# Kernel tuning notes

Hardware: AMD Instinct MI355X
Metric: run time of the kernel (lower is better)

The kernel has to match this reference:

```python
import jax, jax.numpy as jnp
import numpy as np

B, L, E, H, CDIM = 512, 64, 256, 256, 64
NEG = -1e9  # stand-in for -inf mask fill (keeps grads nan-free; probs underflow to 0)
C_EXPL = 10.0  # tanh_exploration


def setup_inputs():
    key = jax.random.key(0)
    ks = jax.random.split(key, 24)
    rn = lambda k, s: jax.random.normal(k, s, jnp.float32) * 0.05
    return {
        'decoder_input': rn(ks[0], (B, E)),
        'embedded_inputs': rn(ks[1], (L, B, E)),
        'h0': rn(ks[2], (B, H)),
        'c0': rn(ks[3], (B, H)),
        'context': rn(ks[4], (L, B, H)),
        'courier_fea': rn(ks[5], (B, CDIM)),
        'init_mask': jnp.zeros((B, L), dtype=bool),
        # LSTMCell params (torch gate order i,f,g,o)
        'W_ih': rn(ks[6], (4 * H, E)), 'W_hh': rn(ks[7], (4 * H, H)),
        'b_ih': rn(ks[8], (4 * H,)), 'b_hh': rn(ks[9], (4 * H,)),
        # merge_linear
        'Wm': rn(ks[10], (H, H + CDIM)), 'bm': rn(ks[11], (H,)),
        # pointer attention
        'Wq_p': rn(ks[12], (H, H)), 'bq_p': rn(ks[13], (H,)),
        'Wr_p': rn(ks[14], (H, H)), 'br_p': rn(ks[15], (H,)),
        'v_p': rn(ks[16], (H,)),
        # glimpse attention
        'Wq_g': rn(ks[17], (H, H)), 'bq_g': rn(ks[18], (H,)),
        'Wr_g': rn(ks[19], (H, H)), 'br_g': rn(ks[20], (H,)),
        'v_g': rn(ks[21], (H,)),
    }


def _attn_scores(q_lin, e, v, use_tanh):
    # q_lin: [B,H], e: [B,H,L], v: [H] -> u: [B,L]
    u = jnp.einsum('h,bhl->bl', v, jnp.tanh(q_lin[:, :, None] + e))
    return C_EXPL * jnp.tanh(u) if use_tanh else u


def _forward(decoder_input, embedded_inputs, h0, c0, context, courier_fea,
             W_ih, W_hh, b_ih, b_hh, Wm, bm,
             Wq_p, bq_p, Wr_p, br_p, v_p,
             Wq_g, bq_g, Wr_g, br_g, v_g, init_mask):
    Ln, Bn = context.shape[0], context.shape[1]
    # conv1d(kernel=1) projection of encoder refs; constant over steps -> precompute
    e_g = jnp.einsum('oh,lbh->bol', Wr_g, context) + br_g[None, :, None]  # [B,H,L]
    e_p = jnp.einsum('oh,lbh->bol', Wr_p, context) + br_p[None, :, None]
    rows = jnp.arange(Bn)

    def update_mask(mask, sel):
        m = mask.at[rows, sel].set(True)
        all_true = m.all(axis=1)
        return m.at[:, -1].set(jnp.where(all_true, False, m[:, -1]))

    def step(carry, t):
        h, c, mask, idxs, x = carry
        mask = jnp.where(t == 0, mask, update_mask(mask, jnp.clip(idxs, 0)))
        # LSTMCell
        gates = x @ W_ih.T + b_ih + h @ W_hh.T + b_hh
        i_, f_, g_, o_ = jnp.split(gates, 4, axis=1)
        c = jax.nn.sigmoid(f_) * c + jax.nn.sigmoid(i_) * jnp.tanh(g_)
        h = jax.nn.sigmoid(o_) * jnp.tanh(c)
        # merge hidden with courier features
        gl = jnp.concatenate([h, courier_fea], axis=1) @ Wm.T + bm
        # one glimpse (n_glimpses=1), masked
        lg = _attn_scores(gl @ Wq_g.T + bq_g, e_g, v_g, use_tanh=False)
        lg = jnp.where(mask, NEG, lg)
        gl = jnp.einsum('bhl,bl->bh', e_g, jax.nn.softmax(lg, axis=1))
        # pointer logits (C*tanh), masked
        lp = _attn_scores(gl @ Wq_p.T + bq_p, e_p, v_p, use_tanh=True)
        lp = jnp.where(mask, NEG, lp)
        log_p = jax.nn.log_softmax(lp, axis=1)  # [B,L]
        new_idxs = jnp.argmax(log_p, axis=1).astype(jnp.int32)  # greedy decode
        new_x = embedded_inputs[new_idxs, rows, :]  # gather next input [B,E]
        return (h, c, mask, new_idxs, new_x), (log_p, new_idxs)

    init = (h0, c0, init_mask, jnp.full((Bn,), -1, jnp.int32), decoder_input)
    _, (log_ps, sels) = jax.lax.scan(step, init, jnp.arange(Ln))
    return jnp.swapaxes(log_ps, 0, 1), jnp.swapaxes(sels, 0, 1)  # [B,L,L], [B,L]


def reference(decoder_input, embedded_inputs, h0, c0, context, courier_fea, init_mask,
              W_ih, W_hh, b_ih, b_hh, Wm, bm,
              Wq_p, bq_p, Wr_p, br_p, v_p,
              Wq_g, bq_g, Wr_g, br_g, v_g):
    return _forward(decoder_input, embedded_inputs, h0, c0, context, courier_fea,
                    W_ih, W_hh, b_ih, b_hh, Wm, bm,
                    Wq_p, bq_p, Wr_p, br_p, v_p,
                    Wq_g, bq_g, Wr_g, br_g, v_g, init_mask)
```

## Files before the change

### kernel.cpp

```cpp
#include <hip/hip_runtime.h>
#include <cstdint>
#include <cstddef>

#define NEGV -1000000000.0f

__device__ __forceinline__ float fsigm(float x) {
  return 1.0f / (1.0f + __expf(-x));
}
__device__ __forceinline__ float ftanh(float x) {
  x = fminf(x, 30.0f);
  const float e = __expf(2.0f * x);
  return (e - 1.0f) / (e + 1.0f);
}

__global__ __launch_bounds__(256, 2) void gemm2_k(
    const float* __restrict__ A0, const float* __restrict__ W2,
    const float* __restrict__ b2, float* __restrict__ Cg,
    float* __restrict__ Cp)
{
  __shared__ float As[16][136];
  __shared__ float Ws[2][16][72];
  const int bn = blockIdx.x << 6;
  const int bm = blockIdx.y << 7;
  const int t  = threadIdx.x;
  const int ty = t >> 4, tx = t & 15;
  const int ar = t >> 1, ac = (t & 1) << 3;
  const int wr = t >> 2, wc = (t & 3) << 2;
  const float* arow = A0 + (size_t)(bm + ar) * 256 + ac;
  float acc[2][8][4] = {};
  for (int k0 = 0; k0 < 256; k0 += 16) {
    const float4 a0 = *(const float4*)(arow + k0);
    const float4 a1 = *(const float4*)(arow + k0 + 4);
    As[ac + 0][ar] = a0.x; As[ac + 1][ar] = a0.y; As[ac + 2][ar] = a0.z; As[ac + 3][ar] = a0.w;
    As[ac + 4][ar] = a1.x; As[ac + 5][ar] = a1.y; As[ac + 6][ar] = a1.z; As[ac + 7][ar] = a1.w;
#pragma unroll
    for (int s = 0; s < 2; ++s) {
      const float4 wv = *(const float4*)(W2 + (size_t)(s * 256 + bn + wr) * 256 + k0 + wc);
      Ws[s][wc + 0][wr] = wv.x; Ws[s][wc + 1][wr] = wv.y;
      Ws[s][wc + 2][wr] = wv.z; Ws[s][wc + 3][wr] = wv.w;
    }
    __syncthreads();
#pragma unroll
    for (int k = 0; k < 16; ++k) {
      const float4 a0v = *(const float4*)&As[k][ty << 3];
      const float4 a1v = *(const float4*)&As[k][(ty << 3) + 4];
      const float am[8] = {a0v.x, a0v.y, a0v.z, a0v.w, a1v.x, a1v.y, a1v.z, a1v.w};
#pragma unroll
      for (int s = 0; s < 2; ++s) {
        const float4 wv = *(const float4*)&Ws[s][k][tx << 2];
#pragma unroll
        for (int i = 0; i < 8; ++i) {
          acc[s][i][0] += am[i] * wv.x;
          acc[s][i][1] += am[i] * wv.y;
          acc[s][i][2] += am[i] * wv.z;
          acc[s][i][3] += am[i] * wv.w;
        }
      }
    }
    __syncthreads();
  }
  const int cn = bn + (tx << 2);
  const float4 bg = *(const float4*)(b2 + cn);
  const float4 bp = *(const float4*)(b2 + 256 + cn);
#pragma unroll
  for (int i = 0; i < 8; ++i) {
    const size_t row = ((size_t)(bm + (ty << 3) + i)) << 8;
    float4 o;
    o.x = acc[0][i][0] + bg.x; o.y = acc[0][i][1] + bg.y;
    o.z = acc[0][i][2] + bg.z; o.w = acc[0][i][3] + bg.w;
    *(float4*)(Cg + row + cn) = o;
    o.x = acc[1][i][0] + bp.x; o.y = acc[1][i][1] + bp.y;
    o.z = acc[1][i][2] + bp.z; o.w = acc[1][i][3] + bp.w;
    *(float4*)(Cp + row + cn) = o;
  }
}

__global__ __launch_bounds__(256) void gates_lstm_k(
    const float* __restrict__ x, const float* __restrict__ hin,
    const float* __restrict__ Wcat, const float* __restrict__ bcat,
    const float* __restrict__ cin, float* __restrict__ cnew,
    float* __restrict__ hnew)
{
  __shared__ __align__(16) float As[16][36];
  __shared__ __align__(16) float Ws[32][68];
  const int bn = blockIdx.x << 6;
  const int bm = blockIdx.y << 4;
  const int t  = threadIdx.x;
  const int ty = t >> 4, tx = t & 15;
  const int ar = t >> 4, ak = (t & 15) << 1;
  const int wr = t >> 2, wk = (t & 3) << 3;
  const float* wrow = Wcat + ((size_t)(bn + wr) << 9);
  const int arow = bm + ar;
  float acc0 = 0.f, acc1 = 0.f, acc2 = 0.f, acc3 = 0.f;
  for (int k0 = 0; k0 < 512; k0 += 32) {
    const int kk = k0 + ak;
    float2 av;
    if (kk < 256) av = *(const float2*)(x   + ((size_t)arow << 8) + kk);
    else          av = *(const float2*)(hin + ((size_t)arow << 8) + (kk - 256));
    const float4 w0 = *(const float4*)(wrow + k0 + wk);
    const float4 w1 = *(const float4*)(wrow + k0 + wk + 4);
    *(float2*)&As[ar][ak] = av;
    Ws[wk + 0][wr] = w0.x; Ws[wk + 1][wr] = w0.y; Ws[wk + 2][wr] = w0.z; Ws[wk + 3][wr] = w0.w;
    Ws[wk + 4][wr] = w1.x; Ws[wk + 5][wr] = w1.y; Ws[wk + 6][wr] = w1.z; Ws[wk + 7][wr] = w1.w;
    __syncthreads();
#pragma unroll
    for (int k = 0; k < 32; ++k) {
      const float a  = As[ty][k];
      const float4 w = *(const float4*)&Ws[k][tx << 2];
      acc0 += a * w.x; acc1 += a * w.y; acc2 += a * w.z; acc3 += a * w.w;
    }
    __syncthreads();
  }
  const float4 bb = *(const float4*)(bcat + bn + (tx << 2));
  const int jc = (bn >> 2) + tx;
  const int m  = bm + ty;
  const float ig = fsigm(acc0 + bb.x);
  const float fg = fsigm(acc1 + bb.y);
  const float gg = ftanh(acc2 + bb.z);
  const float og = fsigm(acc3 + bb.w);
  const float c  = fg * cin[(m << 8) + jc] + ig * gg;
  const float h  = og * ftanh(c);
  cnew[(m << 8) + jc] = c;
  hnew[(m << 8) + jc] = h;
}

__global__ __launch_bounds__(512) void step_attn_k(
    const float* __restrict__ h, const float* __restrict__ e2g,
    const float* __restrict__ e2p, const float* __restrict__ Wq1T4,
    const float* __restrict__ Wqp4, const float* __restrict__ qcour,
    const float* __restrict__ bqp, const float* __restrict__ vg,
    const float* __restrict__ vp, unsigned long long* __restrict__ mask,
    int* __restrict__ idxb, const float* __restrict__ emb,
    float* __restrict__ out_logp, float* __restrict__ out_sel,
    float* __restrict__ xb, int t)
{
  const int b = blockIdx.x, tid = threadIdx.x;
  __shared__ __align__(16) float hs[256], qgs[256], qps[256], gls[256];
  __shared__ __align__(16) float vgs[256], vps[256];
  __shared__ __align__(16) float glp[8][256];
  __shared__ __align__(16) float part[512];
  __shared__ float us[64], mxs[8], zws[8];
  __shared__ unsigned long long ms;
  __shared__ int bsel;
  if (tid < 256) {
    hs[tid]  = h[(b << 8) + tid];
    vgs[tid] = vg[tid];
    vps[tid] = vp[tid];
  }
  if (tid == 0) {
    unsigned long long m = mask[b];
    if (t > 0) {
      int s = idxb[b]; if (s < 0) s = 0;
      m |= (1ULL << s);
      if (m == ~0ULL) m &= ~(1ULL << 63);
      mask[b] = m;
    }
    ms = m;
  }
  __syncthreads();
  const unsigned long long mm = ms;
  const int w = tid >> 6, lane = tid & 63;
  const int o = tid & 255, kh = tid >> 8;

  {
    float acc = (kh == 0) ? qcour[(b << 8) + o] : 0.f;
    const float4* wp = (const float4*)Wq1T4 + o;
    const int kc0 = kh << 5;
#pragma unroll 8
    for (int kc = kc0; kc < kc0 + 32; ++kc) {
      const float4 wv = wp[kc << 8];
      const float4 h4 = *(const float4*)&hs[kc << 2];
      acc += wv.x * h4.x + wv.y * h4.y + wv.z * h4.z + wv.w * h4.w;
    }
    part[tid] = acc;
  }
  __syncthreads();
  if (tid < 256) qgs[tid] = part[tid] + part[tid + 256];
  __syncthreads();

  {
    const float4 q4 = *(const float4*)&qgs[lane << 2];
    const float4 v4 = *(const float4*)&vgs[lane << 2];
    const float* ebase = e2g + ((size_t)b << 8) + (lane << 2);
    float g0 = 0.f, g1 = 0.f, g2 = 0.f, g3 = 0.f;
    float mxw = -1e30f, zw = 0.f;
    for (int li = 0; li < 8; ++li) {
      const int l = (w << 3) + li;
      const float4 e4 = *(const float4*)(ebase + ((size_t)l << 17));
      float s = v4.x * ftanh(q4.x + e4.x) + v4.y * ftanh(q4.y + e4.y)
              + v4.z * ftanh(q4.z + e4.z) + v4.w * ftanh(q4.w + e4.w);
#pragma unroll
      for (int off = 32; off; off >>= 1) s += __shfl_xor(s, off, 64);
      if (!((mm >> l) & 1ULL)) {
        const float nm   = fmaxf(mxw, s);
        const float corr = __expf(mxw - nm);
        const float wl   = __expf(s - nm);
        zw = zw * corr + wl;
        g0 = g0 * corr + wl * e4.x; g1 = g1 * corr + wl * e4.y;
        g2 = g2 * corr + wl * e4.z; g3 = g3 * corr + wl * e4.w;
        mxw = nm;
      }
    }
    glp[w][(lane << 2) + 0] = g0; glp[w][(lane << 2) + 1] = g1;
    glp[w][(lane << 2) + 2] = g2; glp[w][(lane << 2) + 3] = g3;
    if (lane == 0) { mxs[w] = mxw; zws[w] = zw; }
  }
  __syncthreads();
  if (tid < 256) {
    float MX = mxs[0];
#pragma unroll
    for (int ww = 1; ww < 8; ++ww) MX = fmaxf(MX, mxs[ww]);
    float Z = 0.f, go = 0.f;
#pragma unroll
    for (int ww = 0; ww < 8; ++ww) {
      const float sc = __expf(mxs[ww] - MX);
      Z  += sc * zws[ww];
      go += sc * glp[ww][tid];
    }
    gls[tid] = go / Z;
  }
  __syncthreads();

  {
    float acc = (kh == 0) ? bqp[o] : 0.f;
    const float4* wp = (const float4*)Wqp4 + o;
    const int kc0 = kh << 5;
#pragma unroll 8
    for (int kc = kc0; kc < kc0 + 32; ++kc) {
      const float4 wv = wp[kc << 8];
      const float4 h4 = *(const float4*)&gls[kc << 2];
      acc += wv.x * h4.x + wv.y * h4.y + wv.z * h4.z + wv.w * h4.w;
    }
    part[tid] = acc;
  }
  __syncthreads();
  if (tid < 256) qps[tid] = part[tid] + part[tid + 256];
  __syncthreads();

  {
    const float4 q4 = *(const float4*)&qps[lane << 2];
    const float4 v4 = *(const float4*)&vps[lane << 2];
    const float* ebase = e2p + ((size_t)b << 8) + (lane << 2);
    for (int li = 0; li < 8; ++li) {
      const int l = (w << 3) + li;
      const float4 e4 = *(const float4*)(ebase + ((size_t)l << 17));
      float s = v4.x * ftanh(q4.x + e4.x) + v4.y * ftanh(q4.y + e4.y)
              + v4.z * ftanh(q4.z + e4.z) + v4.w * ftanh(q4.w + e4.w);
#pragma unroll
      for (int off = 32; off; off >>= 1) s += __shfl_xor(s, off, 64);
      if (lane == 0) us[l] = ((mm >> l) & 1ULL) ? NEGV : 10.0f * ftanh(s);
    }
  }
  __syncthreads();
  if (tid < 64) {
    const float xv = us[tid];
    float mx = xv;
#pragma unroll
    for (int off = 32; off; off >>= 1) mx = fmaxf(mx, __shfl_xor(mx, off, 64));
    const float sh = xv - mx;
    const float ev = __expf(sh);
    float sum = ev;
#pragma unroll
    for (int off = 32; off; off >>= 1) sum += __shfl_xor(sum, off, 64);
    const float lp = sh - __logf(sum);
    out_logp[((size_t)b << 12) + (t << 6) + tid] = lp;
    float bv = lp; int bi = tid;
#pragma unroll
    for (int off = 32; off; off >>= 1) {
      const float ov = __shfl_xor(bv, off, 64);
      const int   oi = __shfl_xor(bi, off, 64);
      if (ov > bv || (ov == bv && oi < bi)) { bv = ov; bi = oi; }
    }
    if (tid == 0) { idxb[b] = bi; out_sel[(b << 6) + t] = (float)bi; bsel = bi; }
  }
  __syncthreads();
  if (tid < 256) xb[(b << 8) + tid] = emb[(((size_t)(bsel << 9) + b) << 8) + tid];
}

__global__ __launch_bounds__(256) void init_k(
    const float* __restrict__ dec, const float* __restrict__ h0,
    const float* __restrict__ c0, float* __restrict__ xb,
    float* __restrict__ hb, float* __restrict__ cb,
    unsigned long long* __restrict__ mask, int* __restrict__ idxb)
{
  const int i = blockIdx.x * 256 + threadIdx.x;
  xb[i] = dec[i]; hb[i] = h0[i]; cb[i] = c0[i];
  if (i < 512) { mask[i] = 0ULL; idxb[i] = -1; }
}

__global__ __launch_bounds__(256) void prep_wcat_k(
    const float* __restrict__ Wih, const float* __restrict__ Whh,
    const float* __restrict__ bih, const float* __restrict__ bhh,
    float* __restrict__ Wcat, float* __restrict__ bcat)
{
  const int id = blockIdx.x * 256 + threadIdx.x;
  const int n = id >> 9, k = id & 511;
  const int r = ((n & 3) << 8) + (n >> 2);
  Wcat[id] = (k < 256) ? Wih[(r << 8) + k] : Whh[(r << 8) + (k - 256)];
  if (id < 1024) {
    const int rr = ((id & 3) << 8) + (id >> 2);
    bcat[id] = bih[rr] + bhh[rr];
  }
}

__global__ __launch_bounds__(256) void prep_wfused_k(
    const float* __restrict__ Wqg, const float* __restrict__ Wm,
    const float* __restrict__ bm, const float* __restrict__ bqg,
    float* __restrict__ Wf, float* __restrict__ bf)
{
  const int id = blockIdx.x * 256 + threadIdx.x;
  const int o = id / 320, j = id % 320;
  float acc = 0.f;
  for (int tt = 0; tt < 256; ++tt) acc += Wqg[(o << 8) + tt] * Wm[tt * 320 + j];
  Wf[id] = acc;
  if (id < 256) {
    float a2 = 0.f;
    for (int tt = 0; tt < 256; ++tt) a2 += Wqg[(id << 8) + tt] * bm[tt];
    bf[id] = a2 + bqg[id];
  }
}

__global__ __launch_bounds__(256) void prep_wq1t4_k(
    const float* __restrict__ Wf, float* __restrict__ Wq1T4)
{
  const int id = blockIdx.x * 256 + threadIdx.x;
  const int k = id >> 8, o = id & 255;
  Wq1T4[((k >> 2) << 10) + (o << 2) + (k & 3)] = Wf[o * 320 + k];
}

__global__ __launch_bounds__(256) void prep_wqp4_k(
    const float* __restrict__ Wqp, float* __restrict__ Wqp4)
{
  const int id = blockIdx.x * 256 + threadIdx.x;
  const int k = id >> 8, o = id & 255;
  Wqp4[((k >> 2) << 10) + (o << 2) + (k & 3)] = Wqp[(o << 8) + k];
}

__global__ __launch_bounds__(256) void prep_qcour_k(
    const float* __restrict__ Wf, const float* __restrict__ bf,
    const float* __restrict__ cour, float* __restrict__ qcour)
{
  const int b = blockIdx.x, o = threadIdx.x;
  __shared__ float cs[64];
  if (o < 64) cs[o] = cour[(b << 6) + o];
  __syncthreads();
  float acc = bf[o];
#pragma unroll 8
  for (int k = 0; k < 64; ++k) acc += Wf[o * 320 + 256 + k] * cs[k];
  qcour[(b << 8) + o] = acc;
}

__global__ __launch_bounds__(256) void prep_w2copy_k(
    const float* __restrict__ Wrg, const float* __restrict__ Wrp,
    const float* __restrict__ brg, const float* __restrict__ brp,
    float* __restrict__ W2, float* __restrict__ b2)
{
  const int id = blockIdx.x * 256 + threadIdx.x;
  W2[id] = (id < 65536) ? Wrg[id] : Wrp[id - 65536];
  if (id < 256) b2[id] = brg[id];
  else if (id < 512) b2[id] = brp[id - 256];
}

extern "C" void kernel_launch(void* const* d_in, const int* in_sizes, int n_in,
                              void* d_out, int out_size, void* d_ws, size_t ws_size,
                              hipStream_t stream)
{
  const float* dec   = (const float*)d_in[0];
  const float* emb   = (const float*)d_in[1];
  const float* h0    = (const float*)d_in[2];
  const float* c0    = (const float*)d_in[3];
  const float* ctxin = (const float*)d_in[4];
  const float* cour  = (const float*)d_in[5];
  const float* Wih   = (const float*)d_in[7];
  const float* Whh   = (const float*)d_in[8];
  const float* bih   = (const float*)d_in[9];
  const float* bhh   = (const float*)d_in[10];
  const float* Wm    = (const float*)d_in[11];
  const float* bm    = (const float*)d_in[12];
  const float* Wqp   = (const float*)d_in[13];
  const float* bqp   = (const float*)d_in[14];
  const float* Wrp   = (const float*)d_in[15];
  const float* brp   = (const float*)d_in[16];
  const float* vp    = (const float*)d_in[17];
  const float* Wqg   = (const float*)d_in[18];
  const float* bqg   = (const float*)d_in[19];
  const float* Wrg   = (const float*)d_in[20];
  const float* brg   = (const float*)d_in[21];
  const float* vg    = (const float*)d_in[22];

  float* ws = (float*)d_ws;
  float* e2g    = ws + 0;
  float* e2p    = ws + 8388608;
  float* W2     = ws + 16777216;
  float* b2     = ws + 16908288;
  float* Wcat   = ws + 16908800;
  float* bcat   = ws + 17433088;
  float* Wfused = ws + 17434112;
  float* bfused = ws + 17516032;
  float* Wq1T4  = ws + 17516288;
  float* Wqp4   = ws + 17581824;
  float* qcour  = ws + 17647360;
  float* hb0    = ws + 17778432;
  float* hb1    = ws + 17909504;
  float* cb0    = ws + 18040576;
  float* cb1    = ws + 18171648;
  float* xb     = ws + 18302720;
  unsigned long long* maskb = (unsigned long long*)(ws + 18433792);
  int* idxb     = (int*)(ws + 18434816);

  float* out_logp = (float*)d_out;
  float* out_sel  = (float*)d_out + 2097152;

  init_k<<<512, 256, 0, stream>>>(dec, h0, c0, xb, hb0, cb0, maskb, idxb);
  prep_wcat_k<<<2048, 256, 0, stream>>>(Wih, Whh, bih, bhh, Wcat, bcat);
  prep_wfused_k<<<320, 256, 0, stream>>>(Wqg, Wm, bm, bqg, Wfused, bfused);
  prep_wq1t4_k<<<256, 256, 0, stream>>>(Wfused, Wq1T4);
  prep_wqp4_k<<<256, 256, 0, stream>>>(Wqp, Wqp4);
  prep_qcour_k<<<512, 256, 0, stream>>>(Wfused, bfused, cour, qcour);
  prep_w2copy_k<<<512, 256, 0, stream>>>(Wrg, Wrp, brg, brp, W2, b2);
  gemm2_k<<<dim3(4, 256), 256, 0, stream>>>(ctxin, W2, b2, e2g, e2p);

  for (int t = 0; t < 64; ++t) {
    float* hcur = (t & 1) ? hb1 : hb0;
    float* hnew = (t & 1) ? hb0 : hb1;
    float* ccur = (t & 1) ? cb1 : cb0;
    float* cnew = (t & 1) ? cb0 : cb1;
    gates_lstm_k<<<dim3(16, 32), 256, 0, stream>>>(xb, hcur, Wcat, bcat,
                                                   ccur, cnew, hnew);
    step_attn_k<<<512, 512, 0, stream>>>(hnew, e2g, e2p, Wq1T4, Wqp4, qcour,
                                         bqp, vg, vp, maskb, idxb, emb,
                                         out_logp, out_sel, xb, t);
  }
}
```

Before: 3.187 ms.

## Prefetch global loads into registers across GEMM tiles and attention phases

Both GEMM kernels now load the next k-tile from global memory into registers while the current tile is computed from shared memory, a register double-buffering scheme. The gemm2 grid is transposed so consecutive blocks walk the M dimension. The step attention kernel issues its e2g loads before the query matvec and its e2p loads before the glimpse reduction, so the memory latency overlaps earlier compute. This raises register pressure, which could reduce occupancy in the 512-thread attention kernel.

```diff
diff --git a/kernel.cpp b/kernel.cpp
--- a/kernel.cpp
+++ b/kernel.cpp
@@ -20,26 +20,34 @@
 {
   __shared__ float As[16][136];
   __shared__ float Ws[2][16][72];
-  const int bn = blockIdx.x << 6;
-  const int bm = blockIdx.y << 7;
+  const int bm = blockIdx.x << 7;
+  const int bn = blockIdx.y << 6;
   const int t  = threadIdx.x;
   const int ty = t >> 4, tx = t & 15;
   const int ar = t >> 1, ac = (t & 1) << 3;
   const int wr = t >> 2, wc = (t & 3) << 2;
   const float* arow = A0 + (size_t)(bm + ar) * 256 + ac;
+  const float* w0row = W2 + (size_t)(bn + wr) * 256 + wc;
+  const float* w1row = W2 + (size_t)(256 + bn + wr) * 256 + wc;
   float acc[2][8][4] = {};
+  float4 a0 = *(const float4*)(arow + 0);
+  float4 a1 = *(const float4*)(arow + 4);
+  float4 wv0 = *(const float4*)(w0row + 0);
+  float4 wv1 = *(const float4*)(w1row + 0);
   for (int k0 = 0; k0 < 256; k0 += 16) {
-    const float4 a0 = *(const float4*)(arow + k0);
-    const float4 a1 = *(const float4*)(arow + k0 + 4);
     As[ac + 0][ar] = a0.x; As[ac + 1][ar] = a0.y; As[ac + 2][ar] = a0.z; As[ac + 3][ar] = a0.w;
     As[ac + 4][ar] = a1.x; As[ac + 5][ar] = a1.y; As[ac + 6][ar] = a1.z; As[ac + 7][ar] = a1.w;
-#pragma unroll
-    for (int s = 0; s < 2; ++s) {
-      const float4 wv = *(const float4*)(W2 + (size_t)(s * 256 + bn + wr) * 256 + k0 + wc);
-      Ws[s][wc + 0][wr] = wv.x; Ws[s][wc + 1][wr] = wv.y;
-      Ws[s][wc + 2][wr] = wv.z; Ws[s][wc + 3][wr] = wv.w;
-    }
+    Ws[0][wc + 0][wr] = wv0.x; Ws[0][wc + 1][wr] = wv0.y;
+    Ws[0][wc + 2][wr] = wv0.z; Ws[0][wc + 3][wr] = wv0.w;
+    Ws[1][wc + 0][wr] = wv1.x; Ws[1][wc + 1][wr] = wv1.y;
+    Ws[1][wc + 2][wr] = wv1.z; Ws[1][wc + 3][wr] = wv1.w;
     __syncthreads();
+    if (k0 < 240) {
+      a0  = *(const float4*)(arow + k0 + 16);
+      a1  = *(const float4*)(arow + k0 + 20);
+      wv0 = *(const float4*)(w0row + k0 + 16);
+      wv1 = *(const float4*)(w1row + k0 + 16);
+    }
 #pragma unroll
     for (int k = 0; k < 16; ++k) {
       const float4 a0v = *(const float4*)&As[k][ty << 3];
@@ -91,18 +99,25 @@
   const int wr = t >> 2, wk = (t & 3) << 3;
   const float* wrow = Wcat + ((size_t)(bn + wr) << 9);
   const int arow = bm + ar;
+  const int jc = (bn >> 2) + tx;
+  const int m  = bm + ty;
+  const float cin_v = cin[(m << 8) + jc];
   float acc0 = 0.f, acc1 = 0.f, acc2 = 0.f, acc3 = 0.f;
+  float2 av = *(const float2*)(x + ((size_t)arow << 8) + ak);
+  float4 w0 = *(const float4*)(wrow + wk);
+  float4 w1 = *(const float4*)(wrow + wk + 4);
   for (int k0 = 0; k0 < 512; k0 += 32) {
-    const int kk = k0 + ak;
-    float2 av;
-    if (kk < 256) av = *(const float2*)(x   + ((size_t)arow << 8) + kk);
-    else          av = *(const float2*)(hin + ((size_t)arow << 8) + (kk - 256));
-    const float4 w0 = *(const float4*)(wrow + k0 + wk);
-    const float4 w1 = *(const float4*)(wrow + k0 + wk + 4);
     *(float2*)&As[ar][ak] = av;
     Ws[wk + 0][wr] = w0.x; Ws[wk + 1][wr] = w0.y; Ws[wk + 2][wr] = w0.z; Ws[wk + 3][wr] = w0.w;
     Ws[wk + 4][wr] = w1.x; Ws[wk + 5][wr] = w1.y; Ws[wk + 6][wr] = w1.z; Ws[wk + 7][wr] = w1.w;
     __syncthreads();
+    if (k0 < 480) {
+      const int kk = k0 + 32 + ak;
+      if (kk < 256) av = *(const float2*)(x   + ((size_t)arow << 8) + kk);
+      else          av = *(const float2*)(hin + ((size_t)arow << 8) + (kk - 256));
+      w0 = *(const float4*)(wrow + k0 + 32 + wk);
+      w1 = *(const float4*)(wrow + k0 + 32 + wk + 4);
+    }
 #pragma unroll
     for (int k = 0; k < 32; ++k) {
       const float a  = As[ty][k];
@@ -112,13 +127,11 @@
     __syncthreads();
   }
   const float4 bb = *(const float4*)(bcat + bn + (tx << 2));
-  const int jc = (bn >> 2) + tx;
-  const int m  = bm + ty;
   const float ig = fsigm(acc0 + bb.x);
   const float fg = fsigm(acc1 + bb.y);
   const float gg = ftanh(acc2 + bb.z);
   const float og = fsigm(acc3 + bb.w);
-  const float c  = fg * cin[(m << 8) + jc] + ig * gg;
+  const float c  = fg * cin_v + ig * gg;
   const float h  = og * ftanh(c);
   cnew[(m << 8) + jc] = c;
   hnew[(m << 8) + jc] = h;
@@ -142,11 +155,20 @@
   __shared__ float us[64], mxs[8], zws[8];
   __shared__ unsigned long long ms;
   __shared__ int bsel;
+  const int w = tid >> 6, lane = tid & 63;
+  const int o = tid & 255, kh = tid >> 8;
+
   if (tid < 256) {
     hs[tid]  = h[(b << 8) + tid];
     vgs[tid] = vg[tid];
     vps[tid] = vp[tid];
   }
+  const float* ebg = e2g + ((size_t)b << 8) + (lane << 2);
+  float4 eg[8];
+#pragma unroll
+  for (int li = 0; li < 8; ++li)
+    eg[li] = *(const float4*)(ebg + ((size_t)((w << 3) + li) << 17));
+
   if (tid == 0) {
     unsigned long long m = mask[b];
     if (t > 0) {
@@ -159,8 +181,6 @@
   }
   __syncthreads();
   const unsigned long long mm = ms;
-  const int w = tid >> 6, lane = tid & 63;
-  const int o = tid & 255, kh = tid >> 8;
 
   {
     float acc = (kh == 0) ? qcour[(b << 8) + o] : 0.f;
@@ -181,12 +201,12 @@
   {
     const float4 q4 = *(const float4*)&qgs[lane << 2];
     const float4 v4 = *(const float4*)&vgs[lane << 2];
-    const float* ebase = e2g + ((size_t)b << 8) + (lane << 2);
     float g0 = 0.f, g1 = 0.f, g2 = 0.f, g3 = 0.f;
     float mxw = -1e30f, zw = 0.f;
+#pragma unroll
     for (int li = 0; li < 8; ++li) {
       const int l = (w << 3) + li;
-      const float4 e4 = *(const float4*)(ebase + ((size_t)l << 17));
+      const float4 e4 = eg[li];
       float s = v4.x * ftanh(q4.x + e4.x) + v4.y * ftanh(q4.y + e4.y)
               + v4.z * ftanh(q4.z + e4.z) + v4.w * ftanh(q4.w + e4.w);
 #pragma unroll
@@ -205,6 +225,11 @@
     glp[w][(lane << 2) + 2] = g2; glp[w][(lane << 2) + 3] = g3;
     if (lane == 0) { mxs[w] = mxw; zws[w] = zw; }
   }
+  const float* ebp = e2p + ((size_t)b << 8) + (lane << 2);
+  float4 ep[8];
+#pragma unroll
+  for (int li = 0; li < 8; ++li)
+    ep[li] = *(const float4*)(ebp + ((size_t)((w << 3) + li) << 17));
   __syncthreads();
   if (tid < 256) {
     float MX = mxs[0];
@@ -240,10 +265,10 @@
   {
     const float4 q4 = *(const float4*)&qps[lane << 2];
     const float4 v4 = *(const float4*)&vps[lane << 2];
-    const float* ebase = e2p + ((size_t)b << 8) + (lane << 2);
+#pragma unroll
     for (int li = 0; li < 8; ++li) {
       const int l = (w << 3) + li;
-      const float4 e4 = *(const float4*)(ebase + ((size_t)l << 17));
+      const float4 e4 = ep[li];
       float s = v4.x * ftanh(q4.x + e4.x) + v4.y * ftanh(q4.y + e4.y)
               + v4.z * ftanh(q4.z + e4.z) + v4.w * ftanh(q4.w + e4.w);
 #pragma unroll
@@ -418,7 +443,7 @@
   prep_wqp4_k<<<256, 256, 0, stream>>>(Wqp, Wqp4);
   prep_qcour_k<<<512, 256, 0, stream>>>(Wfused, bfused, cour, qcour);
   prep_w2copy_k<<<512, 256, 0, stream>>>(Wrg, Wrp, brg, brp, W2, b2);
-  gemm2_k<<<dim3(4, 256), 256, 0, stream>>>(ctxin, W2, b2, e2g, e2p);
+  gemm2_k<<<dim3(256, 4), 256, 0, stream>>>(ctxin, W2, b2, e2g, e2p);
 
   for (int t = 0; t < 64; ++t) {
     float* hcur = (t & 1) ? hb1 : hb0;
```

New measurement: 3.998 ms. +25.5%, slower.
